# Kernel optimization log

Hardware: AMD Instinct MI355X
Metric: run time of the kernel (lower is better)

Reference implementation:

```python
import jax, jax.numpy as jnp
import numpy as np
import math

B, C, H, W = 4, 64, 64, 64
N_HEAD = 1
GROUPS = 16
EPS = 1e-5


def dwconv_block(x, w, b, pad):
    # ReflectionPad2d(pad) -> depthwise Conv2d -> LeakyReLU(0.01)
    xp = jnp.pad(x, ((0, 0), (0, 0), (pad, pad), (pad, pad)), mode='reflect')
    y = jax.lax.conv_general_dilated(
        xp, w, window_strides=(1, 1), padding='VALID',
        dimension_numbers=('NCHW', 'OIHW', 'NCHW'),
        feature_group_count=x.shape[1])
    y = y + b[None, :, None, None]
    return jax.nn.leaky_relu(y, 0.01)


def group_norm(x, w, b):
    bb, c, h, ww = x.shape
    xg = x.reshape(bb, GROUPS, c // GROUPS, h, ww)
    mu = xg.mean(axis=(2, 3, 4), keepdims=True)
    var = xg.var(axis=(2, 3, 4), keepdims=True)
    xg = (xg - mu) * jax.lax.rsqrt(var + EPS)
    return xg.reshape(bb, c, h, ww) * w[None, :, None, None] + b[None, :, None, None]


def attention(q, k, v):
    # q,k,v: [B, n_head, head_dim, H, W]; softmax over flattened key grid
    bb, n, d, h, ww = q.shape
    qf = q.reshape(bb, n, d, h * ww)
    kf = k.reshape(bb, n, d, h * ww)
    vf = v.reshape(bb, n, d, h * ww)
    scores = jnp.einsum('bndq,bndk->bnqk', qf, kf) / math.sqrt(C)
    attn = jax.nn.softmax(scores, axis=-1)  # [B,n,HW,HW]
    out = jnp.einsum('bnqk,bndk->bndq', attn, vf)
    return out.reshape(bb, n * d, h, ww)


def conv1x1(x, w, b=None):
    y = jnp.einsum('oc,bchw->bohw', w, x)
    if b is not None:
        y = y + b[None, :, None, None]
    return y


def setup_inputs() -> dict:
    key = jax.random.key(0)
    ks = jax.random.split(key, 16)
    s = lambda fan: 1.0 / math.sqrt(fan)
    return {
        'inputs': jax.random.normal(ks[0], (B, C, H, W), jnp.float32),
        'dw1_w': jax.random.normal(ks[1], (C, 1, 3, 3), jnp.float32) * s(9),
        'dw1_b': jnp.zeros((C,), jnp.float32),
        'dw2_w': jax.random.normal(ks[2], (C, 1, 5, 5), jnp.float32) * s(25),
        'dw2_b': jnp.zeros((C,), jnp.float32),
        'gnA_w': jnp.ones((C,), jnp.float32),
        'gnA_b': jnp.zeros((C,), jnp.float32),
        'gnB_w': jnp.ones((C,), jnp.float32),
        'gnB_b': jnp.zeros((C,), jnp.float32),
        'qkvA_w': jax.random.normal(ks[3], (3 * C, C), jnp.float32) * s(C),
        'qkvB_w': jax.random.normal(ks[4], (3 * C, C), jnp.float32) * s(C),
        'outA_w': jax.random.normal(ks[5], (C, C), jnp.float32) * s(C),
        'outA_b': jnp.zeros((C,), jnp.float32),
        'outB_w': jax.random.normal(ks[6], (C, C), jnp.float32) * s(C),
        'outB_b': jnp.zeros((C,), jnp.float32),
    }


def reference(inputs, dw1_w, dw1_b, dw2_w, dw2_b, gnA_w, gnA_b, gnB_w, gnB_b,
              qkvA_w, qkvB_w, outA_w, outA_b, outB_w, outB_b):
    x = dwconv_block(inputs, dw1_w, dw1_b, pad=1)
    y = dwconv_block(inputs, dw2_w, dw2_b, pad=2)
    head_dim = C // N_HEAD

    x_A = group_norm(x, gnA_w, gnA_b)
    qkv_A = conv1x1(x_A, qkvA_w).reshape(B, N_HEAD, head_dim * 3, H, W)
    qA, kA, vA = jnp.split(qkv_A, 3, axis=2)

    x_B = group_norm(y, gnB_w, gnB_b)
    qkv_B = conv1x1(x_B, qkvB_w).reshape(B, N_HEAD, head_dim * 3, H, W)
    qB, kB, vB = jnp.split(qkv_B, 3, axis=2)

    # branch A: queries from B, keys/values from A
    out_A = conv1x1(attention(qB, kA, vA), outA_w, outA_b) + x_A
    # branch B: queries from A, keys/values from B
    out_B = conv1x1(attention(qA, kB, vB), outB_w, outB_b) + x_B
    return jnp.concatenate((out_A, out_B), axis=1)
```

## Files before the change

### kernel.cpp

```cpp
#include <hip/hip_runtime.h>
#include <hip/hip_bf16.h>

#define HW 4096
#define CCH 64

typedef __attribute__((ext_vector_type(8))) short short8;
typedef __attribute__((ext_vector_type(4))) float f32x4;
typedef unsigned short ushort_t;
typedef unsigned long long u64;

#define SCALE_Q 0.18033688f

__device__ __forceinline__ unsigned short f2b(float f) {
  unsigned u = __float_as_uint(f);
  return (unsigned short)((u + 0x7fff + ((u >> 16) & 1)) >> 16);
}
__device__ __forceinline__ float b2f(ushort_t u) {
  return __uint_as_float(((unsigned)u) << 16);
}
__device__ __forceinline__ unsigned cvtpk(float lo, float hi) {
  unsigned r;
  asm volatile("v_cvt_pk_bf16_f32 %0, %1, %2" : "=v"(r) : "v"(lo), "v"(hi));
  return r;
}
__device__ __forceinline__ void gload16(const void* g, void* l) {
  __builtin_amdgcn_global_load_lds(
      (const __attribute__((address_space(1))) unsigned int*)g,
      (__attribute__((address_space(3))) unsigned int*)l, 16, 0, 0);
}

__global__ void __launch_bounds__(256) k_dwconv(
    const float* __restrict__ in, const float* __restrict__ w1, const float* __restrict__ b1,
    const float* __restrict__ w2, const float* __restrict__ b2,
    ushort_t* __restrict__ x, ushort_t* __restrict__ y, float* __restrict__ sums) {
  __shared__ float sm[20 * 68];
  __shared__ float red[4][4];
  const int bc = blockIdx.x >> 2;
  const int strip = blockIdx.x & 3;
  const int r0 = strip * 16;
  const int c = bc & 63;
  const float* p = in + bc * HW;
  const int tid = threadIdx.x;
  for (int idx = tid; idx < 20 * 68; idx += 256) {
    int r = r0 + idx / 68 - 2, cc = idx % 68 - 2;
    r = r < 0 ? -r : (r > 63 ? 126 - r : r);
    cc = cc < 0 ? -cc : (cc > 63 ? 126 - cc : cc);
    sm[idx] = p[r * 64 + cc];
  }
  float w1r[9], w2r[25];
  for (int i = 0; i < 9; i++) w1r[i] = w1[c * 9 + i];
  for (int i = 0; i < 25; i++) w2r[i] = w2[c * 25 + i];
  const float bb1 = b1[c], bb2 = b2[c];
  __syncthreads();

  const int i = tid >> 4;
  const int j0 = (tid & 15) * 4;
  float rv[5][8];
  for (int u = 0; u < 5; u++) {
    *(f32x4*)&rv[u][0] = *(const f32x4*)&sm[(i + u) * 68 + j0];
    *(f32x4*)&rv[u][4] = *(const f32x4*)&sm[(i + u) * 68 + j0 + 4];
  }
  float a1[4], a2[4];
  for (int px = 0; px < 4; px++) {
    float s2 = bb2;
    for (int u = 0; u < 5; u++)
      for (int v = 0; v < 5; v++) s2 += w2r[u * 5 + v] * rv[u][px + v];
    float s1 = bb1;
    for (int u = 0; u < 3; u++)
      for (int v = 0; v < 3; v++) s1 += w1r[u * 3 + v] * rv[u + 1][px + 1 + v];
    a1[px] = s1 > 0.f ? s1 : 0.01f * s1;
    a2[px] = s2 > 0.f ? s2 : 0.01f * s2;
  }
  ushort_t t1[4], t2[4];
  for (int px = 0; px < 4; px++) { t1[px] = f2b(a1[px]); t2[px] = f2b(a2[px]); }
  const int off = bc * HW + (r0 + i) * 64 + j0;
  *(u64*)(x + off) = *(const u64*)t1;
  *(u64*)(y + off) = *(const u64*)t2;

  float s1 = 0, q1 = 0, s2 = 0, q2 = 0;
  for (int px = 0; px < 4; px++) {
    s1 += a1[px]; q1 += a1[px] * a1[px];
    s2 += a2[px]; q2 += a2[px] * a2[px];
  }
  for (int o = 1; o < 64; o <<= 1) {
    s1 += __shfl_xor(s1, o); q1 += __shfl_xor(q1, o);
    s2 += __shfl_xor(s2, o); q2 += __shfl_xor(q2, o);
  }
  if ((tid & 63) == 0) {
    red[tid >> 6][0] = s1; red[tid >> 6][1] = q1;
    red[tid >> 6][2] = s2; red[tid >> 6][3] = q2;
  }
  __syncthreads();
  if (tid == 0) {
    float r4[4];
    for (int k = 0; k < 4; k++)
      r4[k] = red[0][k] + red[1][k] + red[2][k] + red[3][k];
    sums[bc * 8 + strip * 2 + 0] = r4[0];
    sums[bc * 8 + strip * 2 + 1] = r4[1];
    sums[2048 + bc * 8 + strip * 2 + 0] = r4[2];
    sums[2048 + bc * 8 + strip * 2 + 1] = r4[3];
  }
}

__device__ __forceinline__ void gn_coeffs(
    const float* __restrict__ sums, int b, int br, int ch,
    const float* __restrict__ gw, const float* __restrict__ gb,
    float& sc_out, float& sh_out) {
  const float* pp = sums + br * 2048 + (b * 64 + ch) * 8;
  const f32x4 pa = *(const f32x4*)pp;
  const f32x4 pb = *(const f32x4*)(pp + 4);
  float s = pa[0] + pa[2] + pb[0] + pb[2];
  float ss = pa[1] + pa[3] + pb[1] + pb[3];
  s += __shfl_xor(s, 1); ss += __shfl_xor(ss, 1);
  s += __shfl_xor(s, 2); ss += __shfl_xor(ss, 2);
  const float mu = s * (1.f / 16384.f);
  const float var = ss * (1.f / 16384.f) - mu * mu;
  const float rsig = rsqrtf(var + 1e-5f);
  const float a = rsig * gw[ch];
  sc_out = a;
  sh_out = gb[ch] - mu * a;
}

__global__ void __launch_bounds__(256) k_qkv(
    const ushort_t* __restrict__ xbf, const ushort_t* __restrict__ ybf,
    const float* __restrict__ sums,
    const float* __restrict__ gwA, const float* __restrict__ gbA,
    const float* __restrict__ gwB, const float* __restrict__ gbB,
    const float* __restrict__ wA, const float* __restrict__ wB,
    ushort_t* __restrict__ Qt, ushort_t* __restrict__ Kt, ushort_t* __restrict__ Vv) {
  __shared__ float scs[64], shs[64];
  const int id = blockIdx.x * 256 + threadIdx.x;
  const int pg = id & 1023;
  const int chunk = (id >> 10) % 24;
  const int h = id / (1024 * 24);
  const int b = h >> 1, br = h & 1;
  if (threadIdx.x < 64) {
    float a, sh;
    gn_coeffs(sums, b, br, threadIdx.x, br ? gwB : gwA, br ? gbB : gbA, a, sh);
    scs[threadIdx.x] = a;
    shs[threadIdx.x] = sh;
  }
  __syncthreads();
  const ushort_t* X = (br ? ybf : xbf) + b * (CCH * HW);
  const float* W = br ? wB : wA;
  const int pix0 = pg * 4;
  const int r0 = chunk * 8;
  float acc[8][4];
  for (int r = 0; r < 8; r++) for (int p = 0; p < 4; p++) acc[r][p] = 0.f;
  for (int cc = 0; cc < 64; cc++) {
    const float sc = scs[cc], sh = shs[cc];
    const u64 raw = *(const u64*)(X + cc * HW + pix0);
    f32x4 xv;
    for (int p = 0; p < 4; p++)
      xv[p] = b2f((ushort_t)(raw >> (16 * p))) * sc + sh;
    for (int r = 0; r < 8; r++) {
      float wv = W[(r0 + r) * 64 + cc];
      for (int p = 0; p < 4; p++) acc[r][p] += wv * xv[p];
    }
  }
  if (chunk < 16) {
    ushort_t* dst = chunk < 8 ? Qt : Kt;
    const float qs = chunk < 8 ? SCALE_Q : 1.0f;
    const int d0 = (chunk & 7) * 8;
    for (int p = 0; p < 4; p++) {
      short8 v;
      for (int r = 0; r < 8; r++) v[r] = (short)f2b(acc[r][p] * qs);
      *(short8*)(dst + ((h * HW + pix0 + p) << 6) + d0) = v;
    }
  } else {
    const int d0 = (chunk - 16) * 8;
    for (int r = 0; r < 8; r++) {
      ushort_t tmp[4];
      for (int p = 0; p < 4; p++) tmp[p] = f2b(acc[r][p]);
      *(u64*)(Vv + (h * CCH + d0 + r) * HW + pix0) = *(const u64*)tmp;
    }
  }
}

__global__ void __launch_bounds__(256, 3) k_attn(
    const ushort_t* __restrict__ Qt, const ushort_t* __restrict__ Kt,
    const ushort_t* __restrict__ Vv,
    const float* __restrict__ oAw, const float* __restrict__ oAb,
    const float* __restrict__ oBw, const float* __restrict__ oBb,
    const ushort_t* __restrict__ xbf, const ushort_t* __restrict__ ybf,
    const float* __restrict__ sums,
    const float* __restrict__ gwA, const float* __restrict__ gbA,
    const float* __restrict__ gwB, const float* __restrict__ gbB,
    float* __restrict__ out) {
  __shared__ __align__(16) char lds[41472];
  const int h = blockIdx.x >> 6;
  const int qt = blockIdx.x & 63;
  const int b = h >> 1, br = h & 1;
  const int qh = b * 2 + (1 - br);
  const int tid = threadIdx.x;
  const int lane = tid & 63;
  const int wave = tid >> 6;
  const int q = lane & 15, g = lane >> 4;
  const int qbase = qt * 64 + wave * 16;

  float* scs = (float*)(lds + 40960);
  float* shs = scs + 64;
  if (tid < 64) {
    float a, sh;
    gn_coeffs(sums, b, br, tid, br ? gwB : gwA, br ? gbB : gbA, a, sh);
    scs[tid] = a;
    shs[tid] = sh;
  }

  const ushort_t* Qp = Qt + ((qh * HW + qbase + q) << 6);
  const short8 qf0 = *(const short8*)(Qp + g * 8);
  const short8 qf1 = *(const short8*)(Qp + 32 + g * 8);

  const ushort_t* Kh = Kt + ((u64)h * HW << 6);
  const ushort_t* Vh = Vv + (u64)h * (CCH * HW);
  const ushort_t* gk[2];
  const ushort_t* gv[2];
  for (int j = 0; j < 2; j++) {
    const int idx = j * 256 + tid;
    const int rr = idx >> 3, cc = (idx & 7) ^ (rr & 7);
    gk[j] = Kh + (rr << 6) + (cc << 3);
    gv[j] = Vh + rr * HW + (cc << 3);
  }
  char* lK = lds + (tid << 4);
  char* lV = lds + 8192 + (tid << 4);

  float m_run = -1e30f;
  f32x4 o[4] = {};
  f32x4 accl = {};
  char* wp = lds + 32768 + wave * 2048 + (q << 7);
  const int sw = (q & 7) << 4;
  short8 ones;
  for (int j = 0; j < 8; j++) ones[j] = (short)0x3F80;

  for (int j = 0; j < 2; j++) gload16(gk[j], lK + j * 4096);
  for (int j = 0; j < 2; j++) gload16(gv[j], lV + j * 4096);

#pragma unroll 1
  for (int it = 0; it < 64; ++it) {
    if (it < 63) {
      const int nb = (it + 1) & 1;
      for (int j = 0; j < 2; j++)
        gload16(gk[j] + (it + 1) * 4096, lK + nb * 16384 + j * 4096);
      for (int j = 0; j < 2; j++)
        gload16(gv[j] + (it + 1) * 64, lV + nb * 16384 + j * 4096);
      asm volatile("s_waitcnt vmcnt(4)" ::: "memory");
    } else {
      asm volatile("s_waitcnt vmcnt(0)" ::: "memory");
    }
    __builtin_amdgcn_s_barrier();

    const char* kb = lds + (it & 1) * 16384;
    const char* vb = kb + 8192;
    short8 ka[4][2], va[4][2];
    for (int c = 0; c < 4; c++)
      for (int s = 0; s < 2; s++)
        ka[c][s] = *(const short8*)(kb + ((c * 16 + q) << 7) +
                                    (((s * 4 + g) ^ (q & 7)) << 4));
    for (int cd = 0; cd < 4; cd++)
      for (int s = 0; s < 2; s++)
        va[cd][s] = *(const short8*)(vb + ((cd * 16 + q) << 7) +
                                     (((s * 4 + g) ^ (q & 7)) << 4));

    f32x4 sa[4];
    for (int c = 0; c < 4; c++) {
      f32x4 zz = {0.f, 0.f, 0.f, 0.f};
      zz = __builtin_amdgcn_mfma_f32_16x16x32_bf16(ka[c][0], qf0, zz, 0, 0, 0);
      sa[c] = __builtin_amdgcn_mfma_f32_16x16x32_bf16(ka[c][1], qf1, zz, 0, 0, 0);
    }
    float m0 = fmaxf(fmaxf(fmaxf(sa[0][0], sa[0][1]), sa[0][2]), sa[0][3]);
    float m1 = fmaxf(fmaxf(fmaxf(sa[1][0], sa[1][1]), sa[1][2]), sa[1][3]);
    float m2 = fmaxf(fmaxf(fmaxf(sa[2][0], sa[2][1]), sa[2][2]), sa[2][3]);
    float m3 = fmaxf(fmaxf(fmaxf(sa[3][0], sa[3][1]), sa[3][2]), sa[3][3]);
    float mloc = fmaxf(fmaxf(m0, m1), fmaxf(m2, m3));
    mloc = fmaxf(mloc, __shfl_xor(mloc, 16));
    mloc = fmaxf(mloc, __shfl_xor(mloc, 32));
    if (!__all(mloc <= m_run + 8.f)) {
      const float mnew = fmaxf(m_run, mloc);
      const float alpha = exp2f(m_run - mnew);
      for (int cd = 0; cd < 4; cd++)
        for (int i = 0; i < 4; i++) o[cd][i] *= alpha;
      for (int i = 0; i < 4; i++) accl[i] *= alpha;
      m_run = mnew;
    }
    u64 pk[4];
    for (int c = 0; c < 4; c++) {
      float p0 = exp2f(sa[c][0] - m_run), p1 = exp2f(sa[c][1] - m_run);
      float p2 = exp2f(sa[c][2] - m_run), p3 = exp2f(sa[c][3] - m_run);
      pk[c] = (u64)cvtpk(p0, p1) | ((u64)cvtpk(p2, p3) << 32);
    }
    for (int c = 0; c < 4; c++)
      *(u64*)(wp + (((c << 5) | (g << 3)) ^ sw)) = pk[c];
    asm volatile("s_waitcnt lgkmcnt(0)" ::: "memory");
    __builtin_amdgcn_sched_barrier(0);
    const short8 pb0 = *(const short8*)(wp + ((g << 4) ^ sw));
    const short8 pb1 = *(const short8*)(wp + ((64 | (g << 4)) ^ sw));
    for (int cd = 0; cd < 4; cd++) {
      o[cd] = __builtin_amdgcn_mfma_f32_16x16x32_bf16(va[cd][0], pb0, o[cd], 0, 0, 0);
      o[cd] = __builtin_amdgcn_mfma_f32_16x16x32_bf16(va[cd][1], pb1, o[cd], 0, 0, 0);
    }
    accl = __builtin_amdgcn_mfma_f32_16x16x32_bf16(ones, pb0, accl, 0, 0, 0);
    accl = __builtin_amdgcn_mfma_f32_16x16x32_bf16(ones, pb1, accl, 0, 0, 0);
    __builtin_amdgcn_s_barrier();
  }

  __syncthreads();
  float* smW = (float*)(lds + wave * 4096);
  const float inv = 1.f / accl[0];
  for (int cd = 0; cd < 4; cd++) {
    f32x4 v;
    for (int i = 0; i < 4; i++) v[i] = o[cd][i] * inv;
    *(f32x4*)(smW + q * 64 + (((cd * 4 + g) ^ q) << 2)) = v;
  }
  asm volatile("s_waitcnt lgkmcnt(0)" ::: "memory");
  __builtin_amdgcn_sched_barrier(0);

  const float* W    = br ? oBw : oAw;
  const float* bias = br ? oBb : oAb;
  const ushort_t* xR = (br ? ybf : xbf) + b * (CCH * HW);
  const int q2 = lane & 15, g2 = lane >> 4;
  const float* smR = (float*)(lds + wave * 4096) + q2 * 64;
  const int pix = qt * 64 + wave * 16 + q2;

  float acc[16];
  for (int oi = 0; oi < 16; oi++) acc[oi] = bias[g2 * 16 + oi];
  for (int c4 = 0; c4 < 16; c4++) {
    const f32x4 Lv = *(const f32x4*)(smR + ((c4 ^ q2) << 2));
    for (int oi = 0; oi < 16; oi++) {
      const f32x4 wv = *(const f32x4*)(W + (g2 * 16 + oi) * 64 + c4 * 4);
      acc[oi] += wv[0] * Lv[0] + wv[1] * Lv[1] + wv[2] * Lv[2] + wv[3] * Lv[3];
    }
  }
  for (int oi = 0; oi < 16; oi++) {
    const int ch = g2 * 16 + oi;
    const float xn = b2f(xR[ch * HW + pix]) * scs[ch] + shs[ch];
    out[(b * 128 + br * 64 + ch) * HW + pix] = acc[oi] + xn;
  }
}

extern "C" void kernel_launch(void* const* d_in, const int* in_sizes, int n_in,
                              void* d_out, int out_size, void* d_ws, size_t ws_size,
                              hipStream_t stream) {
  const float* in   = (const float*)d_in[0];
  const float* dw1w = (const float*)d_in[1];
  const float* dw1b = (const float*)d_in[2];
  const float* dw2w = (const float*)d_in[3];
  const float* dw2b = (const float*)d_in[4];
  const float* gnAw = (const float*)d_in[5];
  const float* gnAb = (const float*)d_in[6];
  const float* gnBw = (const float*)d_in[7];
  const float* gnBb = (const float*)d_in[8];
  const float* qAw  = (const float*)d_in[9];
  const float* qBw  = (const float*)d_in[10];
  const float* oAw  = (const float*)d_in[11];
  const float* oAb  = (const float*)d_in[12];
  const float* oBw  = (const float*)d_in[13];
  const float* oBb  = (const float*)d_in[14];
  float* out = (float*)d_out;

  char* ws = (char*)d_ws;
  ushort_t* xbf = (ushort_t*)ws;
  ushort_t* ybf = xbf + 1048576;
  ushort_t* Qt  = ybf + 1048576;
  ushort_t* Kt  = Qt + 2097152;
  ushort_t* Vv  = Kt + 2097152;
  float* sums   = (float*)(Vv + 2097152);

  k_dwconv<<<1024, 256, 0, stream>>>(in, dw1w, dw1b, dw2w, dw2b, xbf, ybf, sums);
  k_qkv<<<768, 256, 0, stream>>>(xbf, ybf, sums, gnAw, gnAb, gnBw, gnBb,
                                 qAw, qBw, Qt, Kt, Vv);
  k_attn<<<512, 256, 0, stream>>>(Qt, Kt, Vv, oAw, oAb, oBw, oBb,
                                  xbf, ybf, sums, gnAw, gnAb, gnBw, gnBb, out);
}
```

Before: 219.8 us.

## Split KV sequence across wave halves with 128-query tiles and LDS merge

The attention kernel now uses 512-thread blocks, each covering 128 queries. Each wave handles two 16-query groups, so every K/V tile loaded into LDS feeds twice as many MFMAs. The two halves of the block walk disjoint halves of the key range (split-K), and their partial softmax states are merged at the end through LDS with rescaling and shared-memory atomic adds. This halves the block count to 256 and raises LDS use to about 97KB per block, which lowers occupancy and adds a merge step in exchange for less redundant K/V traffic.

```diff
diff --git a/kernel.cpp b/kernel.cpp
--- a/kernel.cpp
+++ b/kernel.cpp
@@ -177,7 +177,64 @@
   }
 }
 
-__global__ void __launch_bounds__(256, 3) k_attn(
+#define STAGE(B, ITN) do {                                              \
+    gload16(gK0 + ((ITN) << 12), lds + (B)*32768 + (tid << 4));         \
+    gload16(gK1 + ((ITN) << 12), lds + (B)*32768 + 16384 + (tid << 4)); \
+    gload16(gV0 + (ITN)*64,      lds + (B)*32768 + 8192  + (tid << 4)); \
+    gload16(gV1 + (ITN)*64,      lds + (B)*32768 + 24576 + (tid << 4)); \
+  } while (0)
+
+#define GROUP(QFA, QFB, MR, O, ACCL, GOFF) {                                   \
+    f32x4 sa[4];                                                               \
+    _Pragma("unroll") for (int c = 0; c < 4; c++) {                            \
+      f32x4 zz = {0.f, 0.f, 0.f, 0.f};                                         \
+      zz = __builtin_amdgcn_mfma_f32_16x16x32_bf16(ka[c][0], QFA, zz, 0,0,0);  \
+      sa[c] = __builtin_amdgcn_mfma_f32_16x16x32_bf16(ka[c][1], QFB, zz, 0,0,0);\
+    }                                                                          \
+    float mloc = sa[0][0];                                                     \
+    _Pragma("unroll") for (int c = 0; c < 4; c++)                              \
+      _Pragma("unroll") for (int i = 0; i < 4; i++)                            \
+        mloc = fmaxf(mloc, sa[c][i]);                                          \
+    mloc = fmaxf(mloc, __shfl_xor(mloc, 16));                                  \
+    mloc = fmaxf(mloc, __shfl_xor(mloc, 32));                                  \
+    if (!__all(mloc <= MR + 8.f)) {                                            \
+      const float mnew = fmaxf(MR, mloc);                                      \
+      const float alpha = exp2f(MR - mnew);                                    \
+      _Pragma("unroll") for (int cd = 0; cd < 4; cd++)                         \
+        _Pragma("unroll") for (int i = 0; i < 4; i++) O[cd][i] *= alpha;       \
+      _Pragma("unroll") for (int i = 0; i < 4; i++) ACCL[i] *= alpha;          \
+      MR = mnew;                                                               \
+    }                                                                          \
+    _Pragma("unroll") for (int c = 0; c < 4; c++) {                            \
+      float p0 = exp2f(sa[c][0]-MR), p1 = exp2f(sa[c][1]-MR);                  \
+      float p2 = exp2f(sa[c][2]-MR), p3 = exp2f(sa[c][3]-MR);                  \
+      u64 pk = (u64)cvtpk(p0, p1) | ((u64)cvtpk(p2, p3) << 32);                \
+      *(u64*)(pwa[c] + GOFF) = pk;                                             \
+    }                                                                          \
+    asm volatile("s_waitcnt lgkmcnt(0)" ::: "memory");                         \
+    __builtin_amdgcn_sched_barrier(0);                                         \
+    const short8 pb0 = *(const short8*)(pra0 + GOFF);                          \
+    const short8 pb1 = *(const short8*)(pra1 + GOFF);                          \
+    _Pragma("unroll") for (int cd = 0; cd < 4; cd++) {                         \
+      O[cd] = __builtin_amdgcn_mfma_f32_16x16x32_bf16(va[cd][0], pb0, O[cd], 0,0,0); \
+      O[cd] = __builtin_amdgcn_mfma_f32_16x16x32_bf16(va[cd][1], pb1, O[cd], 0,0,0); \
+    }                                                                          \
+    ACCL = __builtin_amdgcn_mfma_f32_16x16x32_bf16(ones, pb0, ACCL, 0,0,0);    \
+    ACCL = __builtin_amdgcn_mfma_f32_16x16x32_bf16(ones, pb1, ACCL, 0,0,0);    \
+  }
+
+#define ATTN_BODY(BOFF) {                                                      \
+    short8 ka[4][2], va[4][2];                                                 \
+    _Pragma("unroll") for (int c = 0; c < 4; c++)                              \
+      _Pragma("unroll") for (int sf = 0; sf < 2; sf++) {                       \
+        ka[c][sf] = *(const short8*)(ka_p[c][sf] + (BOFF));                    \
+        va[c][sf] = *(const short8*)(va_p[c][sf] + (BOFF));                    \
+      }                                                                        \
+    GROUP(qf00, qf01, mr0, o0, accl0, 0)                                       \
+    GROUP(qf10, qf11, mr1, o1, accl1, 2048)                                    \
+  }
+
+__global__ void __launch_bounds__(512, 2) k_attn(
     const ushort_t* __restrict__ Qt, const ushort_t* __restrict__ Kt,
     const ushort_t* __restrict__ Vv,
     const float* __restrict__ oAw, const float* __restrict__ oAb,
@@ -187,18 +244,19 @@
     const float* __restrict__ gwA, const float* __restrict__ gbA,
     const float* __restrict__ gwB, const float* __restrict__ gbB,
     float* __restrict__ out) {
-  __shared__ __align__(16) char lds[41472];
-  const int h = blockIdx.x >> 6;
-  const int qt = blockIdx.x & 63;
+  __shared__ __align__(16) char lds[98816];
+  const int h = blockIdx.x >> 5;
+  const int qt = blockIdx.x & 31;
   const int b = h >> 1, br = h & 1;
   const int qh = b * 2 + (1 - br);
   const int tid = threadIdx.x;
   const int lane = tid & 63;
   const int wave = tid >> 6;
+  const int s = wave >> 2;
+  const int t = wave & 3;
   const int q = lane & 15, g = lane >> 4;
-  const int qbase = qt * 64 + wave * 16;
-
-  float* scs = (float*)(lds + 40960);
+
+  float* scs = (float*)(lds + 98304);
   float* shs = scs + 64;
   if (tid < 64) {
     float a, sh;
@@ -207,129 +265,118 @@
     shs[tid] = sh;
   }
 
-  const ushort_t* Qp = Qt + ((qh * HW + qbase + q) << 6);
-  const short8 qf0 = *(const short8*)(Qp + g * 8);
-  const short8 qf1 = *(const short8*)(Qp + 32 + g * 8);
+  const int qb = qt * 128 + t * 32;
+  const ushort_t* Qp = Qt + ((qh * HW + qb + q) << 6);
+  const short8 qf00 = *(const short8*)(Qp + g * 8);
+  const short8 qf01 = *(const short8*)(Qp + 32 + g * 8);
+  const short8 qf10 = *(const short8*)(Qp + 1024 + g * 8);
+  const short8 qf11 = *(const short8*)(Qp + 1024 + 32 + g * 8);
 
   const ushort_t* Kh = Kt + ((u64)h * HW << 6);
   const ushort_t* Vh = Vv + (u64)h * (CCH * HW);
-  const ushort_t* gk[2];
-  const ushort_t* gv[2];
-  for (int j = 0; j < 2; j++) {
-    const int idx = j * 256 + tid;
-    const int rr = idx >> 3, cc = (idx & 7) ^ (rr & 7);
-    gk[j] = Kh + (rr << 6) + (cc << 3);
-    gv[j] = Vh + rr * HW + (cc << 3);
-  }
-  char* lK = lds + (tid << 4);
-  char* lV = lds + 8192 + (tid << 4);
-
-  float m_run = -1e30f;
-  f32x4 o[4] = {};
-  f32x4 accl = {};
-  char* wp = lds + 32768 + wave * 2048 + (q << 7);
+  const int rr = tid >> 3;
+  const int ck = ((tid & 7) ^ (rr & 7)) << 3;
+  const ushort_t* gK0 = Kh + (rr << 6) + ck;
+  const ushort_t* gK1 = Kh + ((2048 + rr) << 6) + ck;
+  const ushort_t* gV0 = Vh + rr * HW + ck;
+  const ushort_t* gV1 = Vh + rr * HW + 2048 + ck;
+
+  const char* kb0 = lds + s * 16384;
+  const char* vb0 = kb0 + 8192;
+  const char* ka_p[4][2];
+  const char* va_p[4][2];
+#pragma unroll
+  for (int c = 0; c < 4; c++)
+#pragma unroll
+    for (int sf = 0; sf < 2; sf++) {
+      const int o16 = ((c * 16 + q) << 7) + (((sf * 4 + g) ^ (q & 7)) << 4);
+      ka_p[c][sf] = kb0 + o16;
+      va_p[c][sf] = vb0 + o16;
+    }
+
+  char* wpq = lds + 65536 + wave * 4096 + (q << 7);
   const int sw = (q & 7) << 4;
+  char* pwa[4];
+#pragma unroll
+  for (int c = 0; c < 4; c++) pwa[c] = wpq + (((c << 5) | (g << 3)) ^ sw);
+  const char* pra0 = wpq + ((g << 4) ^ sw);
+  const char* pra1 = wpq + ((64 | (g << 4)) ^ sw);
+
+  float mr0 = -1e30f, mr1 = -1e30f;
+  f32x4 o0[4] = {}, o1[4] = {};
+  f32x4 accl0 = {}, accl1 = {};
   short8 ones;
+#pragma unroll
   for (int j = 0; j < 8; j++) ones[j] = (short)0x3F80;
 
-  for (int j = 0; j < 2; j++) gload16(gk[j], lK + j * 4096);
-  for (int j = 0; j < 2; j++) gload16(gv[j], lV + j * 4096);
-
+  STAGE(0, 0);
 #pragma unroll 1
-  for (int it = 0; it < 64; ++it) {
-    if (it < 63) {
-      const int nb = (it + 1) & 1;
-      for (int j = 0; j < 2; j++)
-        gload16(gk[j] + (it + 1) * 4096, lK + nb * 16384 + j * 4096);
-      for (int j = 0; j < 2; j++)
-        gload16(gv[j] + (it + 1) * 64, lV + nb * 16384 + j * 4096);
+  for (int p2 = 0; p2 < 16; ++p2) {
+    STAGE(1, 2 * p2 + 1);
+    asm volatile("s_waitcnt vmcnt(4)" ::: "memory");
+    __builtin_amdgcn_s_barrier();
+    ATTN_BODY(0)
+    __builtin_amdgcn_s_barrier();
+    if (p2 < 15) {
+      STAGE(0, 2 * p2 + 2);
       asm volatile("s_waitcnt vmcnt(4)" ::: "memory");
     } else {
       asm volatile("s_waitcnt vmcnt(0)" ::: "memory");
     }
     __builtin_amdgcn_s_barrier();
-
-    const char* kb = lds + (it & 1) * 16384;
-    const char* vb = kb + 8192;
-    short8 ka[4][2], va[4][2];
-    for (int c = 0; c < 4; c++)
-      for (int s = 0; s < 2; s++)
-        ka[c][s] = *(const short8*)(kb + ((c * 16 + q) << 7) +
-                                    (((s * 4 + g) ^ (q & 7)) << 4));
+    ATTN_BODY(32768)
+    __builtin_amdgcn_s_barrier();
+  }
+
+  float* cmA = (float*)(lds + 65536);
+  float* clA = cmA + 256;
+  __syncthreads();
+  if (lane < 16) {
+    cmA[(wave * 2 + 0) * 16 + q] = mr0;  clA[(wave * 2 + 0) * 16 + q] = accl0[0];
+    cmA[(wave * 2 + 1) * 16 + q] = mr1;  clA[(wave * 2 + 1) * 16 + q] = accl1[0];
+  }
+  for (int i = tid; i < 8192; i += 512) ((float*)lds)[i] = 0.f;
+  __syncthreads();
+#pragma unroll
+  for (int grp = 0; grp < 2; grp++) {
+    const float mA = cmA[(t * 2 + grp) * 16 + q];
+    const float mB = cmA[((t + 4) * 2 + grp) * 16 + q];
+    const float lA = clA[(t * 2 + grp) * 16 + q];
+    const float lB = clA[((t + 4) * 2 + grp) * 16 + q];
+    const float M = fmaxf(mA, mB);
+    const float L = exp2f(mA - M) * lA + exp2f(mB - M) * lB;
+    const float scl = exp2f((grp ? mr1 : mr0) - M) / L;
+    float* smW = (float*)(lds + (t * 2 + grp) * 4096);
+#pragma unroll
     for (int cd = 0; cd < 4; cd++)
-      for (int s = 0; s < 2; s++)
-        va[cd][s] = *(const short8*)(vb + ((cd * 16 + q) << 7) +
-                                     (((s * 4 + g) ^ (q & 7)) << 4));
-
-    f32x4 sa[4];
-    for (int c = 0; c < 4; c++) {
-      f32x4 zz = {0.f, 0.f, 0.f, 0.f};
-      zz = __builtin_amdgcn_mfma_f32_16x16x32_bf16(ka[c][0], qf0, zz, 0, 0, 0);
-      sa[c] = __builtin_amdgcn_mfma_f32_16x16x32_bf16(ka[c][1], qf1, zz, 0, 0, 0);
-    }
-    float m0 = fmaxf(fmaxf(fmaxf(sa[0][0], sa[0][1]), sa[0][2]), sa[0][3]);
-    float m1 = fmaxf(fmaxf(fmaxf(sa[1][0], sa[1][1]), sa[1][2]), sa[1][3]);
-    float m2 = fmaxf(fmaxf(fmaxf(sa[2][0], sa[2][1]), sa[2][2]), sa[2][3]);
-    float m3 = fmaxf(fmaxf(fmaxf(sa[3][0], sa[3][1]), sa[3][2]), sa[3][3]);
-    float mloc = fmaxf(fmaxf(m0, m1), fmaxf(m2, m3));
-    mloc = fmaxf(mloc, __shfl_xor(mloc, 16));
-    mloc = fmaxf(mloc, __shfl_xor(mloc, 32));
-    if (!__all(mloc <= m_run + 8.f)) {
-      const float mnew = fmaxf(m_run, mloc);
-      const float alpha = exp2f(m_run - mnew);
-      for (int cd = 0; cd < 4; cd++)
-        for (int i = 0; i < 4; i++) o[cd][i] *= alpha;
-      for (int i = 0; i < 4; i++) accl[i] *= alpha;
-      m_run = mnew;
-    }
-    u64 pk[4];
-    for (int c = 0; c < 4; c++) {
-      float p0 = exp2f(sa[c][0] - m_run), p1 = exp2f(sa[c][1] - m_run);
-      float p2 = exp2f(sa[c][2] - m_run), p3 = exp2f(sa[c][3] - m_run);
-      pk[c] = (u64)cvtpk(p0, p1) | ((u64)cvtpk(p2, p3) << 32);
-    }
-    for (int c = 0; c < 4; c++)
-      *(u64*)(wp + (((c << 5) | (g << 3)) ^ sw)) = pk[c];
-    asm volatile("s_waitcnt lgkmcnt(0)" ::: "memory");
-    __builtin_amdgcn_sched_barrier(0);
-    const short8 pb0 = *(const short8*)(wp + ((g << 4) ^ sw));
-    const short8 pb1 = *(const short8*)(wp + ((64 | (g << 4)) ^ sw));
-    for (int cd = 0; cd < 4; cd++) {
-      o[cd] = __builtin_amdgcn_mfma_f32_16x16x32_bf16(va[cd][0], pb0, o[cd], 0, 0, 0);
-      o[cd] = __builtin_amdgcn_mfma_f32_16x16x32_bf16(va[cd][1], pb1, o[cd], 0, 0, 0);
-    }
-    accl = __builtin_amdgcn_mfma_f32_16x16x32_bf16(ones, pb0, accl, 0, 0, 0);
-    accl = __builtin_amdgcn_mfma_f32_16x16x32_bf16(ones, pb1, accl, 0, 0, 0);
-    __builtin_amdgcn_s_barrier();
-  }
-
-  __syncthreads();
-  float* smW = (float*)(lds + wave * 4096);
-  const float inv = 1.f / accl[0];
-  for (int cd = 0; cd < 4; cd++) {
-    f32x4 v;
-    for (int i = 0; i < 4; i++) v[i] = o[cd][i] * inv;
-    *(f32x4*)(smW + q * 64 + (((cd * 4 + g) ^ q) << 2)) = v;
-  }
-  asm volatile("s_waitcnt lgkmcnt(0)" ::: "memory");
-  __builtin_amdgcn_sched_barrier(0);
+#pragma unroll
+      for (int i = 0; i < 4; i++) {
+        const float v = (grp ? o1[cd][i] : o0[cd][i]) * scl;
+        atomicAdd(&smW[q * 64 + (((cd * 4 + g) ^ q) << 2) + i], v);
+      }
+  }
+  __syncthreads();
 
   const float* W    = br ? oBw : oAw;
   const float* bias = br ? oBb : oAb;
   const ushort_t* xR = (br ? ybf : xbf) + b * (CCH * HW);
   const int q2 = lane & 15, g2 = lane >> 4;
   const float* smR = (float*)(lds + wave * 4096) + q2 * 64;
-  const int pix = qt * 64 + wave * 16 + q2;
+  const int pix = qt * 128 + wave * 16 + q2;
 
   float acc[16];
+#pragma unroll
   for (int oi = 0; oi < 16; oi++) acc[oi] = bias[g2 * 16 + oi];
+#pragma unroll
   for (int c4 = 0; c4 < 16; c4++) {
     const f32x4 Lv = *(const f32x4*)(smR + ((c4 ^ q2) << 2));
+#pragma unroll
     for (int oi = 0; oi < 16; oi++) {
       const f32x4 wv = *(const f32x4*)(W + (g2 * 16 + oi) * 64 + c4 * 4);
       acc[oi] += wv[0] * Lv[0] + wv[1] * Lv[1] + wv[2] * Lv[2] + wv[3] * Lv[3];
     }
   }
+#pragma unroll
   for (int oi = 0; oi < 16; oi++) {
     const int ch = g2 * 16 + oi;
     const float xn = b2f(xR[ch * HW + pix]) * scs[ch] + shs[ch];
@@ -368,6 +415,6 @@
   k_dwconv<<<1024, 256, 0, stream>>>(in, dw1w, dw1b, dw2w, dw2b, xbf, ybf, sums);
   k_qkv<<<768, 256, 0, stream>>>(xbf, ybf, sums, gnAw, gnAb, gnBw, gnBb,
                                  qAw, qBw, Qt, Kt, Vv);
-  k_attn<<<512, 256, 0, stream>>>(Qt, Kt, Vv, oAw, oAb, oBw, oBb,
+  k_attn<<<256, 512, 0, stream>>>(Qt, Kt, Vv, oAw, oAb, oBw, oBb,
                                   xbf, ybf, sums, gnAw, gnAb, gnBw, gnBb, out);
 }
```

After: 224.5 us. 1.02x slower.
